# Kernel optimization log

Hardware: AMD Instinct MI355X
Metric: run time of the kernel (lower is better)

Reference implementation:

```python
import jax, jax.numpy as jnp
import numpy as np

NUM_HEADS = 16
ROPE_BASE = 10000.0
NEG_INF = -1e9


def _layer_norm(x, g, b, eps=1e-5):
    mu = jnp.mean(x, axis=-1, keepdims=True)
    var = jnp.mean(jnp.square(x - mu), axis=-1, keepdims=True)
    return (x - mu) * jax.lax.rsqrt(var + eps) * g + b


def _rope_tables(seq_len, width):
    # theta_i = base^(-2i/width); tables shape (seq_len, width) with [m*theta, m*theta] concat
    theta = jnp.power(ROPE_BASE, -jnp.arange(0, width, 2, dtype=jnp.float32) / width)
    m_theta = jnp.arange(seq_len, dtype=jnp.float32)[:, None] * theta[None, :]
    m_theta = jnp.concatenate([m_theta, m_theta], axis=-1)
    return jnp.cos(m_theta), jnp.sin(m_theta)


def _apply_rope(x, cos, sin):
    # x: (BH, T, D); cos/sin: (T, D)
    half = x.shape[-1] // 2
    rot = jnp.concatenate([-x[..., half:], x[..., :half]], axis=-1)
    return cos[None] * x + sin[None] * rot


def setup_inputs() -> dict:
    key = jax.random.key(0)
    ks = jax.random.split(key, 6)
    T, B, C, F = 2048, 2, 1024, 4096
    s = 0.02
    return {
        "x": jax.random.normal(ks[0], (T, B, C), jnp.float32),
        "in_w": jax.random.normal(ks[1], (3 * C, C), jnp.float32) * s,
        "in_b": jnp.zeros((3 * C,), jnp.float32),
        "out_w": jax.random.normal(ks[2], (C, C), jnp.float32) * s,
        "out_b": jnp.zeros((C,), jnp.float32),
        "ln1_g": jnp.ones((C,), jnp.float32),
        "ln1_b": jnp.zeros((C,), jnp.float32),
        "ln2_g": jnp.ones((C,), jnp.float32),
        "ln2_b": jnp.zeros((C,), jnp.float32),
        "w1": jax.random.normal(ks[3], (F, C), jnp.float32) * s,
        "b1": jnp.zeros((F,), jnp.float32),
        "w2": jax.random.normal(ks[4], (C, F), jnp.float32) * s,
        "b2": jnp.zeros((C,), jnp.float32),
    }


def reference(x, in_w, in_b, out_w, out_b, ln1_g, ln1_b, ln2_g, ln2_b, w1, b1, w2, b2):
    # x: (T, B, C)  fairseq Time x Batch x Channel
    T, B, C = x.shape
    H = NUM_HEADS
    D = C // H

    # --- self-attention block (pre-LN) ---
    residual = x
    h = _layer_norm(x, ln1_g, ln1_b)
    qkv = h @ in_w.T + in_b                       # (T, B, 3C)
    q, k, v = jnp.split(qkv, 3, axis=-1)
    q = q * (D ** -0.5)

    def to_heads(t):  # (T, B, C) -> (B*H, T, D)
        return t.reshape(T, B * H, D).transpose(1, 0, 2)

    q, k, v = to_heads(q), to_heads(k), to_heads(v)
    cos, sin = _rope_tables(T, D)
    q = _apply_rope(q, cos, sin)
    k = _apply_rope(k, cos, sin)

    scores = jnp.einsum("btd,bsd->bts", q, k)     # (B*H, T, T)
    causal = jnp.triu(jnp.ones((T, T), dtype=bool), k=1)
    scores = jnp.where(causal[None], jnp.float32(NEG_INF), scores)
    attn = jax.nn.softmax(scores, axis=-1)
    o = jnp.einsum("bts,bsd->btd", attn, v)       # (B*H, T, D)
    o = o.transpose(1, 0, 2).reshape(T, B, C)
    o = o @ out_w.T + out_b
    x = residual + o

    # --- FFN block (pre-LN) ---
    residual = x
    h = _layer_norm(x, ln2_g, ln2_b)
    h = jax.nn.gelu(h @ w1.T + b1)
    h = h @ w2.T + b2
    return residual + h
```

## Files before the change

kernel.cpp:

```cpp
#include <hip/hip_runtime.h>
#include <hip/hip_bf16.h>
#include <math.h>

#define T_LEN 2048
#define B_SZ  2
#define C_DIM 1024
#define H_NUM 16
#define D_HEAD 64
#define F_DIM 4096
#define NT    (T_LEN * B_SZ)
#define BH    (B_SZ * H_NUM)
#define C3    (3 * C_DIM)

typedef __attribute__((ext_vector_type(8))) short short8v;
typedef __attribute__((ext_vector_type(4))) float f32x4;
typedef __hip_bfloat16 bf16;

__device__ __forceinline__ float bf2f(bf16 v) { return __bfloat162float(v); }
__device__ __forceinline__ bf16  f2bf(float f) { return __float2bfloat16(f); }
__device__ __forceinline__ short f2bfs(float f) { bf16 h = __float2bfloat16(f); return *(short*)&h; }
__device__ __forceinline__ void split2(float v, short& h, short& l) {
    bf16 hb = __float2bfloat16(v);
    bf16 lb = __float2bfloat16(v - __bfloat162float(hb));
    h = *(short*)&hb; l = *(short*)&lb;
}
__device__ __forceinline__ f32x4 mfma16(short8v a, short8v b, f32x4 c) {
    return __builtin_amdgcn_mfma_f32_16x16x32_bf16(a, b, c, 0, 0, 0);
}

__device__ __forceinline__ float block_sum_256(float val, float* sred) {
#pragma unroll
    for (int off = 32; off > 0; off >>= 1)
        val += __shfl_down(val, off, 64);
    int lane = threadIdx.x & 63;
    int wid  = threadIdx.x >> 6;
    if (lane == 0) sred[wid] = val;
    __syncthreads();
    float r = sred[0] + sred[1] + sred[2] + sred[3];
    __syncthreads();
    return r;
}

__global__ __launch_bounds__(256) void split_kernel(const float* __restrict__ src,
                                                    bf16* __restrict__ hi, bf16* __restrict__ lo) {
    int i = blockIdx.x * 256 + threadIdx.x;
    float4 v = ((const float4*)src)[i];
    short4 hv, lv;
    split2(v.x, hv.x, lv.x); split2(v.y, hv.y, lv.y);
    split2(v.z, hv.z, lv.z); split2(v.w, hv.w, lv.w);
    ((short4*)hi)[i] = hv;
    ((short4*)lo)[i] = lv;
}

__global__ __launch_bounds__(256) void ln_split_kernel(const float* __restrict__ x,
                                                       const float* __restrict__ g,
                                                       const float* __restrict__ b,
                                                       bf16* __restrict__ oh, bf16* __restrict__ ol) {
    __shared__ float sred[4];
    int row = blockIdx.x;
    int tid = threadIdx.x;
    const float* xr = x + (size_t)row * C_DIM;
    float4 xv = *(const float4*)(xr + tid * 4);
    float s = xv.x + xv.y + xv.z + xv.w;
    s = block_sum_256(s, sred);
    float mu = s * (1.0f / C_DIM);
    float d0 = xv.x - mu, d1 = xv.y - mu, d2 = xv.z - mu, d3 = xv.w - mu;
    float vs = d0 * d0 + d1 * d1 + d2 * d2 + d3 * d3;
    vs = block_sum_256(vs, sred);
    float rstd = rsqrtf(vs * (1.0f / C_DIM) + 1e-5f);
    float4 gv = *(const float4*)(g + tid * 4);
    float4 bv = *(const float4*)(b + tid * 4);
    float y0 = d0 * rstd * gv.x + bv.x, y1 = d1 * rstd * gv.y + bv.y;
    float y2 = d2 * rstd * gv.z + bv.z, y3 = d3 * rstd * gv.w + bv.w;
    short4 hv, lv;
    split2(y0, hv.x, lv.x); split2(y1, hv.y, lv.y);
    split2(y2, hv.z, lv.z); split2(y3, hv.w, lv.w);
    size_t base = (size_t)row * C_DIM / 4 + tid;
    ((short4*)oh)[base] = hv;
    ((short4*)ol)[base] = lv;
}

template <int EPI, bool ASPLIT, bool OUTBF16>
__global__ __launch_bounds__(256) void gemm_bf16(const bf16* __restrict__ Ah, const bf16* __restrict__ Al,
                                                 const bf16* __restrict__ Bh, const bf16* __restrict__ Bl,
                                                 const float* __restrict__ bias, const float* __restrict__ res,
                                                 float* __restrict__ Cf, bf16* __restrict__ Cb,
                                                 int N, int K) {
    __shared__ __align__(16) short LAh[128 * 32];
    __shared__ __align__(16) short LBh[128 * 32];
    __shared__ __align__(16) short LBl[128 * 32];
    __shared__ __align__(16) short LAl[ASPLIT ? 128 * 32 : 8];
    char* LAhB = (char*)LAh; char* LBhB = (char*)LBh;
    char* LBlB = (char*)LBl; char* LAlB = (char*)LAl;

    int tid = threadIdx.x;
    int w = tid >> 6, l = tid & 63;
    int c = l & 15, g4 = l >> 4;
    int wm = w >> 1, wn = w & 1;
    int bn = blockIdx.x, bm = blockIdx.y;

    f32x4 acc[4][4];
#pragma unroll
    for (int i = 0; i < 4; i++)
#pragma unroll
        for (int j = 0; j < 4; j++) acc[i][j] = (f32x4){0.f, 0.f, 0.f, 0.f};

    int srow = tid >> 2, skc = tid & 3;
    short8v rAh[2], rAl[2], rBh[2], rBl[2];

    auto LOADT = [&](int kt) {
#pragma unroll
        for (int e = 0; e < 2; e++) {
            int row = srow + e * 64;
            size_t ga = (size_t)(bm * 128 + row) * K + kt + skc * 8;
            size_t gb = (size_t)(bn * 128 + row) * K + kt + skc * 8;
            rAh[e] = *(const short8v*)(Ah + ga);
            if (ASPLIT) rAl[e] = *(const short8v*)(Al + ga);
            rBh[e] = *(const short8v*)(Bh + gb);
            rBl[e] = *(const short8v*)(Bl + gb);
        }
    };
    auto STORET = [&]() {
#pragma unroll
        for (int e = 0; e < 2; e++) {
            int row = srow + e * 64;
            int off = row * 64 + 16 * (skc ^ ((row >> 1) & 3));
            *(short8v*)(LAhB + off) = rAh[e];
            if (ASPLIT) *(short8v*)(LAlB + off) = rAl[e];
            *(short8v*)(LBhB + off) = rBh[e];
            *(short8v*)(LBlB + off) = rBl[e];
        }
    };

    LOADT(0);
    for (int kt = 0; kt < K; kt += 32) {
        __syncthreads();
        STORET();
        __syncthreads();
        if (kt + 32 < K) LOADT(kt + 32);

        short8v fah[4], fal[4], fbh[4], fbl[4];
#pragma unroll
        for (int i = 0; i < 4; i++) {
            int row = wm * 64 + i * 16 + c;
            int off = row * 64 + 16 * (g4 ^ ((row >> 1) & 3));
            fah[i] = *(const short8v*)(LAhB + off);
            if (ASPLIT) fal[i] = *(const short8v*)(LAlB + off);
        }
#pragma unroll
        for (int j = 0; j < 4; j++) {
            int row = wn * 64 + j * 16 + c;
            int off = row * 64 + 16 * (g4 ^ ((row >> 1) & 3));
            fbh[j] = *(const short8v*)(LBhB + off);
            fbl[j] = *(const short8v*)(LBlB + off);
        }
#pragma unroll
        for (int i = 0; i < 4; i++)
#pragma unroll
            for (int j = 0; j < 4; j++) {
                f32x4 t = acc[i][j];
                t = mfma16(fah[i], fbl[j], t);
                if (ASPLIT) t = mfma16(fal[i], fbh[j], t);
                t = mfma16(fah[i], fbh[j], t);
                acc[i][j] = t;
            }
    }

#pragma unroll
    for (int i = 0; i < 4; i++)
#pragma unroll
        for (int j = 0; j < 4; j++) {
            int colg = bn * 128 + wn * 64 + j * 16 + c;
            float bv = bias[colg];
#pragma unroll
            for (int r = 0; r < 4; r++) {
                int rowg = bm * 128 + wm * 64 + i * 16 + g4 * 4 + r;
                float v = acc[i][j][r] + bv;
                if (EPI == 1) {
                    float t = tanhf(0.7978845608028654f * (v + 0.044715f * v * v * v));
                    v = 0.5f * v * (1.0f + t);
                } else if (EPI == 2) {
                    v += res[(size_t)rowg * N + colg];
                }
                if (OUTBF16) Cb[(size_t)rowg * N + colg] = f2bf(v);
                else         Cf[(size_t)rowg * N + colg] = v;
            }
        }
}

__global__ __launch_bounds__(256) void rope_kernel(const bf16* __restrict__ qkv,
                                                   bf16* __restrict__ Q, bf16* __restrict__ K) {
    int idx = blockIdx.x * 256 + threadIdx.x;
    int d  = idx & 31;
    int t  = (idx >> 5) & (T_LEN - 1);
    int bh = idx >> 16;
    int b  = bh >> 4;
    int h  = bh & 15;
    size_t row = (size_t)(t * B_SZ + b) * C3 + h * D_HEAD + d;
    float q0 = bf2f(qkv[row]),          q1 = bf2f(qkv[row + 32]);
    float k0 = bf2f(qkv[row + C_DIM]),  k1 = bf2f(qkv[row + C_DIM + 32]);
    q0 *= 0.125f; q1 *= 0.125f;
    float theta = exp2f((float)d * (-13.287712379549449f / 32.0f));
    float ang = (float)t * theta;
    float sn, cs;
    sincosf(ang, &sn, &cs);
    size_t ob = ((size_t)bh * T_LEN + t) * D_HEAD + d;
    Q[ob]      = f2bf(cs * q0 - sn * q1);
    Q[ob + 32] = f2bf(cs * q1 + sn * q0);
    K[ob]      = f2bf(cs * k0 - sn * k1);
    K[ob + 32] = f2bf(cs * k1 + sn * k0);
}

__global__ __launch_bounds__(256) void vt_kernel(const bf16* __restrict__ qkv, bf16* __restrict__ Vt) {
    __shared__ __align__(16) short L[64 * 64];
    char* LB = (char*)L;
    int qt = blockIdx.x, bh = blockIdx.y;
    int b = bh >> 4, h = bh & 15;
    int tid = threadIdx.x;
    int t0 = qt * 64;
#pragma unroll
    for (int e = 0; e < 2; e++) {
        int t = (tid >> 3) + e * 32, dc = tid & 7;
        short8v v = *(const short8v*)(qkv + (size_t)((t0 + t) * B_SZ + b) * C3 + 2 * C_DIM + h * 64 + dc * 8);
        *(short8v*)(LB + t * 128 + 16 * (dc ^ ((t >> 3) & 7))) = v;
    }
    __syncthreads();
    int d = tid & 63, tcb = tid >> 6;
    short8v v0, v1;
#pragma unroll
    for (int i = 0; i < 8; i++) {
        int t = tcb * 16 + i;
        v0[i] = *(const short*)(LB + t * 128 + 16 * ((d >> 3) ^ ((t >> 3) & 7)) + 2 * (d & 7));
    }
#pragma unroll
    for (int i = 0; i < 8; i++) {
        int t = tcb * 16 + 8 + i;
        v1[i] = *(const short*)(LB + t * 128 + 16 * ((d >> 3) ^ ((t >> 3) & 7)) + 2 * (d & 7));
    }
    bf16* op = Vt + ((size_t)bh * 64 + d) * T_LEN + t0 + tcb * 16;
    *(short8v*)(op)     = v0;
    *(short8v*)(op + 8) = v1;
}

__global__ __launch_bounds__(256) void attn_kernel(const bf16* __restrict__ Qg, const bf16* __restrict__ Kg,
                                                   const bf16* __restrict__ Vt,
                                                   bf16* __restrict__ Ohi, bf16* __restrict__ Olo) {
    __shared__ __align__(16) short Kl[64 * 64];
    __shared__ __align__(16) short Vl[64 * 64];
    __shared__ __align__(16) short Ps[4 * 16 * 64];
    char* KlB = (char*)Kl; char* VlB = (char*)Vl;
    int qt = blockIdx.x, bh = blockIdx.y;
    int tid = threadIdx.x;
    int w = tid >> 6, l = tid & 63;
    int c = l & 15, g4 = l >> 4;
    char* PsB = (char*)Ps + w * 2048;

    int q0 = qt * 64 + w * 16;
    const bf16* Qb = Qg + ((size_t)bh * T_LEN + q0 + c) * 64 + g4 * 8;
    short8v qf0 = *(const short8v*)(Qb);
    short8v qf1 = *(const short8v*)(Qb + 32);

    f32x4 oacc[4];
    float m_r[4], l_r[4];
#pragma unroll
    for (int i = 0; i < 4; i++) { oacc[i] = (f32x4){0.f,0.f,0.f,0.f}; m_r[i] = -1e30f; l_r[i] = 0.f; }

    int skv = tid >> 3, sc8 = tid & 7;
    for (int kt = 0; kt <= qt; kt++) {
        int kv0 = kt * 64;
        short8v kreg[2], vreg[2];
#pragma unroll
        for (int e = 0; e < 2; e++) {
            int rkv = skv + e * 32;
            kreg[e] = *(const short8v*)(Kg + ((size_t)bh * T_LEN + kv0 + rkv) * 64 + sc8 * 8);
            vreg[e] = *(const short8v*)(Vt + ((size_t)bh * 64 + rkv) * T_LEN + kv0 + sc8 * 8);
        }
        __syncthreads();
#pragma unroll
        for (int e = 0; e < 2; e++) {
            int rkv = skv + e * 32;
            *(short8v*)(KlB + rkv * 128 + 16 * (sc8 ^ (rkv & 7))) = kreg[e];
            *(short8v*)(VlB + rkv * 128 + 16 * (sc8 ^ (rkv & 7))) = vreg[e];
        }
        __syncthreads();

        f32x4 s[4];
#pragma unroll
        for (int j = 0; j < 4; j++) s[j] = (f32x4){0.f,0.f,0.f,0.f};
#pragma unroll
        for (int j = 0; j < 4; j++) {
            int row = j * 16 + c;
            short8v kb0 = *(const short8v*)(KlB + row * 128 + 16 * ((g4)     ^ (row & 7)));
            short8v kb1 = *(const short8v*)(KlB + row * 128 + 16 * ((4 + g4) ^ (row & 7)));
            s[j] = mfma16(qf0, kb0, s[j]);
            s[j] = mfma16(qf1, kb1, s[j]);
        }
        if (kt == qt) {
#pragma unroll
            for (int j = 0; j < 4; j++)
#pragma unroll
                for (int r = 0; r < 4; r++)
                    if (j * 16 + c > w * 16 + g4 * 4 + r) s[j][r] = -1e30f;
        }

#pragma unroll
        for (int r = 0; r < 4; r++) {
            float tm = fmaxf(fmaxf(s[0][r], s[1][r]), fmaxf(s[2][r], s[3][r]));
#pragma unroll
            for (int mk = 1; mk < 16; mk <<= 1) tm = fmaxf(tm, __shfl_xor(tm, mk, 64));
            float mnew = fmaxf(m_r[r], tm);
            float sc = __expf(m_r[r] - mnew);
            int q = g4 * 4 + r;
            float rs = 0.f;
#pragma unroll
            for (int j = 0; j < 4; j++) {
                float p = __expf(s[j][r] - mnew);
                rs += p;
                *(short*)(PsB + q * 128 + 16 * ((2 * j + (c >> 3)) ^ (q & 7)) + 2 * (c & 7)) = f2bfs(p);
            }
#pragma unroll
            for (int mk = 1; mk < 16; mk <<= 1) rs += __shfl_xor(rs, mk, 64);
            l_r[r] = l_r[r] * sc + rs;
            m_r[r] = mnew;
#pragma unroll
            for (int jd = 0; jd < 4; jd++) oacc[jd][r] *= sc;
        }
        __syncthreads();

#pragma unroll
        for (int ks = 0; ks < 2; ks++) {
            short8v pa = *(const short8v*)(PsB + c * 128 + 16 * ((ks * 4 + g4) ^ (c & 7)));
#pragma unroll
            for (int jd = 0; jd < 4; jd++) {
                int row = jd * 16 + c;
                short8v vb = *(const short8v*)(VlB + row * 128 + 16 * ((ks * 4 + g4) ^ (row & 7)));
                oacc[jd] = mfma16(pa, vb, oacc[jd]);
            }
        }
    }

    int b = bh >> 4, h = bh & 15;
#pragma unroll
    for (int r = 0; r < 4; r++) {
        float inv = 1.0f / l_r[r];
        int t = qt * 64 + w * 16 + g4 * 4 + r;
        size_t rb = (size_t)(t * B_SZ + b) * C_DIM + h * 64;
#pragma unroll
        for (int jd = 0; jd < 4; jd++) {
            float v = oacc[jd][r] * inv;
            short hs, ls;
            split2(v, hs, ls);
            *(short*)&Ohi[rb + jd * 16 + c] = hs;
            *(short*)&Olo[rb + jd * 16 + c] = ls;
        }
    }
}

extern "C" void kernel_launch(void* const* d_in, const int* in_sizes, int n_in,
                              void* d_out, int out_size, void* d_ws, size_t ws_size,
                              hipStream_t stream) {
    (void)in_sizes; (void)n_in; (void)out_size; (void)ws_size;
    const float* x     = (const float*)d_in[0];
    const float* in_w  = (const float*)d_in[1];
    const float* in_b  = (const float*)d_in[2];
    const float* out_w = (const float*)d_in[3];
    const float* out_b = (const float*)d_in[4];
    const float* ln1_g = (const float*)d_in[5];
    const float* ln1_b = (const float*)d_in[6];
    const float* ln2_g = (const float*)d_in[7];
    const float* ln2_b = (const float*)d_in[8];
    const float* w1    = (const float*)d_in[9];
    const float* b1    = (const float*)d_in[10];
    const float* w2    = (const float*)d_in[11];
    const float* b2    = (const float*)d_in[12];
    float* out = (float*)d_out;
    char* ws = (char*)d_ws;

    const size_t MB = 1 << 20;
    bf16* inw_h  = (bf16*)(ws + 0 * MB);
    bf16* inw_l  = (bf16*)(ws + 6 * MB);
    bf16* outw_h = (bf16*)(ws + 12 * MB);
    bf16* outw_l = (bf16*)(ws + 14 * MB);
    bf16* w1_h   = (bf16*)(ws + 16 * MB);
    bf16* w1_l   = (bf16*)(ws + 24 * MB);
    bf16* w2_h   = (bf16*)(ws + 32 * MB);
    bf16* w2_l   = (bf16*)(ws + 40 * MB);
    bf16* ln1o_h = (bf16*)(ws + 48 * MB);
    bf16* ln1o_l = (bf16*)(ws + 56 * MB);
    bf16* qkv    = (bf16*)(ws + 64 * MB);
    bf16* Qg     = (bf16*)(ws + 88 * MB);
    bf16* Kg     = (bf16*)(ws + 96 * MB);
    bf16* Vt     = (bf16*)(ws + 104 * MB);
    bf16* O_h    = (bf16*)(ws + 48 * MB);
    bf16* O_l    = (bf16*)(ws + 56 * MB);
    float* x2    = (float*)(ws + 112 * MB);
    bf16* h2_h   = (bf16*)(ws + 64 * MB);
    bf16* h2_l   = (bf16*)(ws + 72 * MB);
    bf16* f1     = (bf16*)(ws + 80 * MB);

    split_kernel<<<3072, 256, 0, stream>>>(in_w, inw_h, inw_l);
    split_kernel<<<1024, 256, 0, stream>>>(out_w, outw_h, outw_l);
    split_kernel<<<4096, 256, 0, stream>>>(w1, w1_h, w1_l);
    split_kernel<<<4096, 256, 0, stream>>>(w2, w2_h, w2_l);
    ln_split_kernel<<<NT, 256, 0, stream>>>(x, ln1_g, ln1_b, ln1o_h, ln1o_l);
    gemm_bf16<0, true, true><<<dim3(C3 / 128, NT / 128), 256, 0, stream>>>(
        ln1o_h, ln1o_l, inw_h, inw_l, in_b, nullptr, nullptr, qkv, C3, C_DIM);
    rope_kernel<<<(BH * T_LEN * 32) / 256, 256, 0, stream>>>(qkv, Qg, Kg);
    vt_kernel<<<dim3(T_LEN / 64, BH), 256, 0, stream>>>(qkv, Vt);
    attn_kernel<<<dim3(T_LEN / 64, BH), 256, 0, stream>>>(Qg, Kg, Vt, O_h, O_l);
    gemm_bf16<2, true, false><<<dim3(C_DIM / 128, NT / 128), 256, 0, stream>>>(
        O_h, O_l, outw_h, outw_l, out_b, x, x2, nullptr, C_DIM, C_DIM);
    ln_split_kernel<<<NT, 256, 0, stream>>>(x2, ln2_g, ln2_b, h2_h, h2_l);
    gemm_bf16<1, true, true><<<dim3(F_DIM / 128, NT / 128), 256, 0, stream>>>(
        h2_h, h2_l, w1_h, w1_l, b1, nullptr, nullptr, f1, F_DIM, C_DIM);
    gemm_bf16<2, false, false><<<dim3(C_DIM / 128, NT / 128), 256, 0, stream>>>(
        f1, nullptr, w2_h, w2_l, b2, x2, out, nullptr, C_DIM, F_DIM);
}
```

Baseline: 622.8 us.

## Use direct global-to-LDS async loads in GEMM and reverse attention tile order

The GEMM main loop now stages tiles with global_load_lds, writing straight into the swizzled shared-memory layout instead of going through registers. This removes the register prefetch and the explicit store step, but the load now sits right before the barrier with no double buffering, so its latency is no longer hidden behind compute. Separately, the attention kernel processes query tiles in reverse order so the longest causal blocks are scheduled first, to improve load balance.

```diff
diff --git a/kernel.cpp b/kernel.cpp
--- a/kernel.cpp
+++ b/kernel.cpp
@@ -26,6 +26,11 @@
 }
 __device__ __forceinline__ f32x4 mfma16(short8v a, short8v b, f32x4 c) {
     return __builtin_amdgcn_mfma_f32_16x16x32_bf16(a, b, c, 0, 0, 0);
+}
+__device__ __forceinline__ void async16(const void* g, void* lds) {
+    __builtin_amdgcn_global_load_lds(
+        (const __attribute__((address_space(1))) void*)g,
+        (__attribute__((address_space(3))) void*)lds, 16, 0, 0);
 }
 
 __device__ __forceinline__ float block_sum_256(float val, float* sred) {
@@ -105,39 +110,29 @@
 #pragma unroll
         for (int j = 0; j < 4; j++) acc[i][j] = (f32x4){0.f, 0.f, 0.f, 0.f};
 
-    int srow = tid >> 2, skc = tid & 3;
-    short8v rAh[2], rAl[2], rBh[2], rBl[2];
-
-    auto LOADT = [&](int kt) {
-#pragma unroll
-        for (int e = 0; e < 2; e++) {
-            int row = srow + e * 64;
-            size_t ga = (size_t)(bm * 128 + row) * K + kt + skc * 8;
-            size_t gb = (size_t)(bn * 128 + row) * K + kt + skc * 8;
-            rAh[e] = *(const short8v*)(Ah + ga);
-            if (ASPLIT) rAl[e] = *(const short8v*)(Al + ga);
-            rBh[e] = *(const short8v*)(Bh + gb);
-            rBl[e] = *(const short8v*)(Bl + gb);
+    const bf16* gB[4];
+    gB[0] = Ah + (size_t)bm * 128 * K;
+    gB[1] = Bh + (size_t)bn * 128 * K;
+    gB[2] = Bl + (size_t)bn * 128 * K;
+    gB[3] = ASPLIT ? (Al + (size_t)bm * 128 * K) : gB[0];
+    char* lB[4] = {LAhB, LBhB, LBlB, LAlB};
+    const int NSEG = (ASPLIT ? 4 : 3) * 8;
+    int lr4 = l >> 2, lc4 = l & 3;
+
+    auto STAGE = [&](int kt) {
+#pragma unroll
+        for (int sidx = w; sidx < NSEG; sidx += 4) {
+            int bsel = sidx >> 3, seg = sidx & 7;
+            int r = seg * 16 + lr4;
+            int cs = lc4 ^ ((r >> 1) & 3);
+            const bf16* g = gB[bsel] + (size_t)r * K + kt + cs * 8;
+            async16(g, lB[bsel] + seg * 1024);
         }
     };
-    auto STORET = [&]() {
-#pragma unroll
-        for (int e = 0; e < 2; e++) {
-            int row = srow + e * 64;
-            int off = row * 64 + 16 * (skc ^ ((row >> 1) & 3));
-            *(short8v*)(LAhB + off) = rAh[e];
-            if (ASPLIT) *(short8v*)(LAlB + off) = rAl[e];
-            *(short8v*)(LBhB + off) = rBh[e];
-            *(short8v*)(LBlB + off) = rBl[e];
-        }
-    };
-
-    LOADT(0);
+
     for (int kt = 0; kt < K; kt += 32) {
+        STAGE(kt);
         __syncthreads();
-        STORET();
-        __syncthreads();
-        if (kt + 32 < K) LOADT(kt + 32);
 
         short8v fah[4], fal[4], fbh[4], fbl[4];
 #pragma unroll
@@ -164,6 +159,7 @@
                 t = mfma16(fah[i], fbh[j], t);
                 acc[i][j] = t;
             }
+        __syncthreads();
     }
 
 #pragma unroll
@@ -249,7 +245,8 @@
     __shared__ __align__(16) short Vl[64 * 64];
     __shared__ __align__(16) short Ps[4 * 16 * 64];
     char* KlB = (char*)Kl; char* VlB = (char*)Vl;
-    int qt = blockIdx.x, bh = blockIdx.y;
+    int qt = gridDim.x - 1 - blockIdx.x;
+    int bh = blockIdx.y;
     int tid = threadIdx.x;
     int w = tid >> 6, l = tid & 63;
     int c = l & 15, g4 = l >> 4;
```

Result: slower. 640.2 us (+2.8%).
